# Kernel tuning notes

Measured on AMD Instinct MI355X. Metric: run time of the kernel, lower is better.

Reference implementation:

```python
import jax, jax.numpy as jnp
import numpy as np

NUM_USERS = 100000
NUM_ITEMS = 100000
EMB_DIM = 64
NUM_NODES = NUM_USERS + NUM_ITEMS
NUM_EDGES = 4000000
BATCH = 4096
NUM_LAYERS = 2


def setup_inputs() -> dict:
    key = jax.random.key(0)
    ks = jax.random.split(key, 8)
    user = jax.random.randint(ks[0], (BATCH,), 0, NUM_USERS, dtype=jnp.int64) if jax.config.jax_enable_x64 else jax.random.randint(ks[0], (BATCH,), 0, NUM_USERS, dtype=jnp.int32)
    pos = jax.random.randint(ks[1], (BATCH,), 0, NUM_ITEMS, dtype=jnp.int32)
    neg = jax.random.randint(ks[2], (BATCH,), 0, NUM_ITEMS, dtype=jnp.int32)
    edge_row = jax.random.randint(ks[3], (NUM_EDGES,), 0, NUM_NODES, dtype=jnp.int32)
    edge_col = jax.random.randint(ks[4], (NUM_EDGES,), 0, NUM_NODES, dtype=jnp.int32)
    # normalized adjacency values (degree-normalized in real LightGCN)
    edge_val = jax.random.uniform(ks[5], (NUM_EDGES,), dtype=jnp.float32) * 0.01
    user_emb = jax.random.normal(ks[6], (NUM_USERS, EMB_DIM), dtype=jnp.float32) * 0.01
    item_emb = jax.random.normal(ks[7], (NUM_ITEMS, EMB_DIM), dtype=jnp.float32) * 0.01
    return {"user": user, "pos": pos, "neg": neg,
            "edge_row": edge_row, "edge_col": edge_col, "edge_val": edge_val,
            "user_emb": user_emb, "item_emb": item_emb}


def _spmm(edge_row, edge_col, edge_val, x):
    # out[r] = sum_e val[e] * x[col[e]]  -- sparse adjacency times dense emb
    msgs = edge_val[:, None] * x[edge_col]  # [E, D]
    return jax.ops.segment_sum(msgs, edge_row, num_segments=NUM_NODES)


def reference(user, pos, neg, edge_row, edge_col, edge_val, user_emb, item_emb):
    all_emb = jnp.concatenate([user_emb, item_emb], axis=0)  # [N, D]
    acc = all_emb
    h = all_emb
    for _ in range(NUM_LAYERS):
        h = _spmm(edge_row, edge_col, edge_val, h)
        acc = acc + h
    lightgcn_out = acc / (NUM_LAYERS + 1)  # mean over stacked layer embeddings
    u = lightgcn_out[:NUM_USERS]
    i = lightgcn_out[NUM_USERS:]
    user_latent = u[user]          # [B, D]
    positive_latent = i[pos]       # [B, D]
    negative_latent = i[neg]       # [B, D]
    positive_score = jnp.sum(user_latent * positive_latent, axis=1)
    negative_score = jnp.sum(user_latent * negative_latent, axis=1)
    return positive_score, negative_score
```

## Files before the change

### kernel.cpp

```cpp
#include <hip/hip_runtime.h>
#include <cstdint>
#include <cstddef>

#define NUM_USERS 100000
#define NUM_ITEMS 100000
#define NUM_NODES 200000
#define NUM_EDGES 4000000
#define BATCH     4096
#define EMB       64

#define NB    782
#define CAP   5632
#define CHUNK 16384
#define PTHREADS 1024
#define EPB   16


__device__ __forceinline__ unsigned short f2bf(float f) {
    unsigned u = __float_as_uint(f);
    u = (u + 0x7FFFu + ((u >> 16) & 1u)) >> 16;
    return (unsigned short)u;
}
__device__ __forceinline__ float bf2f(unsigned short b) {
    return __uint_as_float(((unsigned)b) << 16);
}


__global__ void k_cvt(const float* __restrict__ uemb, const float* __restrict__ iemb,
                      unsigned short* __restrict__ xb, int* __restrict__ bcur) {
    int i = blockIdx.x * blockDim.x + threadIdx.x;
    if (i < NB) bcur[i] = i * CAP;
    const int TOT8 = (NUM_NODES * EMB) / 8;
    if (i >= TOT8) return;
    size_t off = (size_t)i * 8;
    const size_t UELEMS = (size_t)NUM_USERS * EMB;
    const float* src = (off < UELEMS) ? (uemb + off) : (iemb + (off - UELEMS));
    float4 f0 = ((const float4*)src)[0];
    float4 f1 = ((const float4*)src)[1];
    ushort4 o0 = make_ushort4(f2bf(f0.x), f2bf(f0.y), f2bf(f0.z), f2bf(f0.w));
    ushort4 o1 = make_ushort4(f2bf(f1.x), f2bf(f1.y), f2bf(f1.z), f2bf(f1.w));
    ((ushort4*)(xb + off))[0] = o0;
    ((ushort4*)(xb + off))[1] = o1;
}


__global__ void k_part1(const int* __restrict__ erow, const int* __restrict__ ecol,
                        const float* __restrict__ eval_, int* __restrict__ bcur,
                        int2* __restrict__ tmp) {
    __shared__ int hist[NB];
    __shared__ int base[NB];
    int t = threadIdx.x;
    int start = blockIdx.x * CHUNK;
    for (int i = t; i < NB; i += PTHREADS) hist[i] = 0;
    __syncthreads();
    int rows[EPB], ranks[EPB];
#pragma unroll
    for (int k = 0; k < EPB; ++k) {
        int e = start + t + k * PTHREADS;
        if (e < NUM_EDGES) {
            int r = erow[e];
            rows[k]  = r;
            ranks[k] = atomicAdd(&hist[r >> 8], 1);
        } else {
            rows[k] = -1;
        }
    }
    __syncthreads();
    for (int i = t; i < NB; i += PTHREADS) {
        int c = hist[i];
        base[i] = c ? atomicAdd(&bcur[i], c) : 0;
    }
    __syncthreads();
#pragma unroll
    for (int k = 0; k < EPB; ++k) {
        int e = start + t + k * PTHREADS;
        if (rows[k] >= 0) {
            int r   = rows[k];
            int bkt = r >> 8;
            int pos = base[bkt] + ranks[k];
            if (pos < (bkt + 1) * CAP)
                tmp[pos] = make_int2(((r & 255) << 24) | ecol[e], __float_as_int(eval_[e]));
        }
    }
}


__global__ void k_part2(const int* __restrict__ bcur, const int2* __restrict__ tmp,
                        int2* __restrict__ epack, int2* __restrict__ rowext) {
    __shared__ int cnt[256];
    __shared__ int sc[256];
    __shared__ int loc[256];
    int b = blockIdx.x, t = threadIdx.x;
    int base_row = b << 8;
    int nrows = min(256, NUM_NODES - base_row);
    int s0 = b * CAP;
    int n = min(bcur[b] - s0, CAP);
    if (t < 256) cnt[t] = 0;
    __syncthreads();
    for (int i = t; i < n; i += 512)
        atomicAdd(&cnt[((unsigned)tmp[s0 + i].x) >> 24], 1);
    __syncthreads();
    int v = 0;
    if (t < 256) { v = cnt[t]; sc[t] = v; }
    __syncthreads();
    for (int off = 1; off < 256; off <<= 1) {
        int add = 0;
        if (t < 256 && t >= off) add = sc[t - off];
        __syncthreads();
        if (t < 256 && t >= off) sc[t] += add;
        __syncthreads();
    }
    if (t < 256) {
        int cur = s0 + sc[t] - v;
        if (t < nrows) rowext[base_row + t] = make_int2(cur, v);
        loc[t] = cur;
    }
    __syncthreads();
    for (int i = t; i < n; i += 512) {
        int2 rec = tmp[s0 + i];
        int pos = atomicAdd(&loc[((unsigned)rec.x) >> 24], 1);
        epack[pos] = make_int2(rec.x & 0xFFFFFF, rec.y);
    }
}


__global__ void k_spmm1(const int2* __restrict__ rowext, const int2* __restrict__ epack,
                        const unsigned short* __restrict__ xb,
                        unsigned short* __restrict__ h1) {
    int wid  = (blockIdx.x * blockDim.x + threadIdx.x) >> 6;
    int lane = threadIdx.x & 63;
    if (wid >= NUM_NODES) return;
    int g = lane >> 4;
    int q = (lane & 15) * 4;
    int2 se = rowext[wid];
    int s = se.x, t = se.x + se.y;
    float a0 = 0.f, a1 = 0.f, a2 = 0.f, a3 = 0.f;
    for (int e = s; e < t; e += 8) {
        int eA = e + g, eB = e + 4 + g;
        int2 pA = epack[eA < t ? eA : s];
        int2 pB = epack[eB < t ? eB : s];
        float vA = (eA < t) ? __int_as_float(pA.y) : 0.f;
        float vB = (eB < t) ? __int_as_float(pB.y) : 0.f;
        ushort4 xA = *(const ushort4*)(xb + (size_t)pA.x * EMB + q);
        ushort4 xB = *(const ushort4*)(xb + (size_t)pB.x * EMB + q);
        a0 = fmaf(vA, bf2f(xA.x), a0); a1 = fmaf(vA, bf2f(xA.y), a1);
        a2 = fmaf(vA, bf2f(xA.z), a2); a3 = fmaf(vA, bf2f(xA.w), a3);
        a0 = fmaf(vB, bf2f(xB.x), a0); a1 = fmaf(vB, bf2f(xB.y), a1);
        a2 = fmaf(vB, bf2f(xB.z), a2); a3 = fmaf(vB, bf2f(xB.w), a3);
    }
    a0 += __shfl_xor(a0, 16, 64); a1 += __shfl_xor(a1, 16, 64);
    a2 += __shfl_xor(a2, 16, 64); a3 += __shfl_xor(a3, 16, 64);
    a0 += __shfl_xor(a0, 32, 64); a1 += __shfl_xor(a1, 32, 64);
    a2 += __shfl_xor(a2, 32, 64); a3 += __shfl_xor(a3, 32, 64);
    if (lane < 16) {
        ushort4 o = make_ushort4(f2bf(a0), f2bf(a1), f2bf(a2), f2bf(a3));
        *(ushort4*)(h1 + (size_t)wid * EMB + q) = o;
    }
}


__device__ __forceinline__ const float* node_ptr(int c, const float* __restrict__ uemb,
                                                 const float* __restrict__ iemb) {
    return (c < NUM_USERS) ? (uemb + (size_t)c * EMB)
                           : (iemb + (size_t)(c - NUM_USERS) * EMB);
}

__global__ void k_final(const int* __restrict__ user, const int* __restrict__ pos,
                        const int* __restrict__ neg,
                        const int2* __restrict__ rowext, const int2* __restrict__ epack,
                        const float* __restrict__ uemb, const float* __restrict__ iemb,
                        const unsigned short* __restrict__ h1, float* __restrict__ out) {
    __shared__ float lds[3 * EMB];
    int b    = blockIdx.x;
    int w    = threadIdx.x >> 6;
    int lane = threadIdx.x & 63;
    int g = lane >> 4;
    int q = (lane & 15) * 4;

    int node;
    if (w == 0)      node = user[b];
    else if (w == 1) node = NUM_USERS + pos[b];
    else             node = NUM_USERS + neg[b];

    int2 se = rowext[node];
    int s = se.x, t = se.x + se.y;
    float a0 = 0.f, a1 = 0.f, a2 = 0.f, a3 = 0.f;
    for (int e = s; e < t; e += 8) {
        int eA = e + g, eB = e + 4 + g;
        int2 pA = epack[eA < t ? eA : s];
        int2 pB = epack[eB < t ? eB : s];
        float vA = (eA < t) ? __int_as_float(pA.y) : 0.f;
        float vB = (eB < t) ? __int_as_float(pB.y) : 0.f;
        ushort4 yA = *(const ushort4*)(h1 + (size_t)pA.x * EMB + q);
        ushort4 yB = *(const ushort4*)(h1 + (size_t)pB.x * EMB + q);
        a0 = fmaf(vA, bf2f(yA.x), a0); a1 = fmaf(vA, bf2f(yA.y), a1);
        a2 = fmaf(vA, bf2f(yA.z), a2); a3 = fmaf(vA, bf2f(yA.w), a3);
        a0 = fmaf(vB, bf2f(yB.x), a0); a1 = fmaf(vB, bf2f(yB.y), a1);
        a2 = fmaf(vB, bf2f(yB.z), a2); a3 = fmaf(vB, bf2f(yB.w), a3);
    }
    a0 += __shfl_xor(a0, 16, 64); a1 += __shfl_xor(a1, 16, 64);
    a2 += __shfl_xor(a2, 16, 64); a3 += __shfl_xor(a3, 16, 64);
    a0 += __shfl_xor(a0, 32, 64); a1 += __shfl_xor(a1, 32, 64);
    a2 += __shfl_xor(a2, 32, 64); a3 += __shfl_xor(a3, 32, 64);

    if (lane < 16) {
        const float* xbp = node_ptr(node, uemb, iemb) + q;
        float4  xd = *(const float4*)xbp;
        ushort4 hn = *(const ushort4*)(h1 + (size_t)node * EMB + q);
        a0 = (a0 + xd.x + bf2f(hn.x)) / 3.0f;
        a1 = (a1 + xd.y + bf2f(hn.y)) / 3.0f;
        a2 = (a2 + xd.z + bf2f(hn.z)) / 3.0f;
        a3 = (a3 + xd.w + bf2f(hn.w)) / 3.0f;
        *(float4*)(lds + w * EMB + q) = make_float4(a0, a1, a2, a3);
    }
    __syncthreads();

    if (w < 2) {
        float prod = lds[lane] * lds[(w + 1) * EMB + lane];
        for (int off = 32; off; off >>= 1) prod += __shfl_xor(prod, off, 64);
        if (lane == 0) out[w * BATCH + b] = prod;
    }
}


extern "C" void kernel_launch(void* const* d_in, const int* in_sizes, int n_in,
                              void* d_out, int out_size, void* d_ws, size_t ws_size,
                              hipStream_t stream) {
    const int*   user  = (const int*)d_in[0];
    const int*   pos   = (const int*)d_in[1];
    const int*   neg   = (const int*)d_in[2];
    const int*   erow  = (const int*)d_in[3];
    const int*   ecol  = (const int*)d_in[4];
    const float* eval_ = (const float*)d_in[5];
    const float* uemb  = (const float*)d_in[6];
    const float* iemb  = (const float*)d_in[7];
    float* out = (float*)d_out;

    char* ws = (char*)d_ws;
    unsigned short* xb = (unsigned short*)(ws);
    unsigned short* h1 = (unsigned short*)(ws + 25600000);
    int2* tmp     = (int2*)(ws + 25600000);
    int2* rowext  = (int2*)(ws + 60833792);
    int*  bcur    = (int*)(ws + 62433792);
    int2* epack   = (int2*)(ws + 62437888);

    k_cvt<<<((NUM_NODES * EMB) / 8 + 255) / 256, 256, 0, stream>>>(uemb, iemb, xb, bcur);

    k_part1<<<(NUM_EDGES + CHUNK - 1) / CHUNK, PTHREADS, 0, stream>>>(erow, ecol, eval_,
                                                                      bcur, tmp);

    k_part2<<<NB, 512, 0, stream>>>(bcur, tmp, epack, rowext);

    k_spmm1<<<(NUM_NODES * 64 + 255) / 256, 256, 0, stream>>>(rowext, epack, xb, h1);

    k_final<<<BATCH, 192, 0, stream>>>(user, pos, neg, rowext, epack,
                                       uemb, iemb, h1, out);
}
```

Before: 352.0 us.

## Compute first-layer SpMM only for rows needed by batch neighbourhoods

The change builds bitmaps marking the batch nodes and then, during the partition pass, the neighbours of those batch nodes. The first-layer SpMM then skips every row that the final gather never reads. It also folds the bf16 conversion kernel into the partition kernel, replaces the bucket-cursor init with a memset, caches records in registers in part2, and splits off the unmasked full-8 edge loop in spmm1. The aim is to cut launches and avoid computing h1 for most of the graph. In exchange it adds a global atomicOr per edge of a marked row and extra bitmap traffic.

Result: no change. 345.2 us (-2.0%).

```diff
diff --git a/kernel.cpp b/kernel.cpp
--- a/kernel.cpp
+++ b/kernel.cpp
@@ -14,6 +14,8 @@
 #define CHUNK 16384
 #define PTHREADS 1024
 #define EPB   16
+#define RPT   11
+#define NWORDS 6250
 
 
 __device__ __forceinline__ unsigned short f2bf(float f) {
@@ -26,33 +28,42 @@
 }
 
 
-__global__ void k_cvt(const float* __restrict__ uemb, const float* __restrict__ iemb,
-                      unsigned short* __restrict__ xb, int* __restrict__ bcur) {
-    int i = blockIdx.x * blockDim.x + threadIdx.x;
-    if (i < NB) bcur[i] = i * CAP;
-    const int TOT8 = (NUM_NODES * EMB) / 8;
-    if (i >= TOT8) return;
-    size_t off = (size_t)i * 8;
-    const size_t UELEMS = (size_t)NUM_USERS * EMB;
-    const float* src = (off < UELEMS) ? (uemb + off) : (iemb + (off - UELEMS));
-    float4 f0 = ((const float4*)src)[0];
-    float4 f1 = ((const float4*)src)[1];
-    ushort4 o0 = make_ushort4(f2bf(f0.x), f2bf(f0.y), f2bf(f0.z), f2bf(f0.w));
-    ushort4 o1 = make_ushort4(f2bf(f1.x), f2bf(f1.y), f2bf(f1.z), f2bf(f1.w));
-    ((ushort4*)(xb + off))[0] = o0;
-    ((ushort4*)(xb + off))[1] = o1;
-}
-
-
-__global__ void k_part1(const int* __restrict__ erow, const int* __restrict__ ecol,
-                        const float* __restrict__ eval_, int* __restrict__ bcur,
+__global__ void k_part1(const int* __restrict__ user, const int* __restrict__ pos,
+                        const int* __restrict__ neg,
+                        const int* __restrict__ erow, const int* __restrict__ ecol,
+                        const float* __restrict__ eval_,
+                        const float* __restrict__ uemb, const float* __restrict__ iemb,
+                        unsigned short* __restrict__ xb,
+                        int* __restrict__ bcur,
+                        unsigned* __restrict__ memb, unsigned* __restrict__ need,
                         int2* __restrict__ tmp) {
     __shared__ int hist[NB];
     __shared__ int base[NB];
     int t = threadIdx.x;
+    int gid = blockIdx.x * PTHREADS + t;
+    for (int i = t; i < NB; i += PTHREADS) hist[i] = 0;
+
+    const int TOT8 = (NUM_NODES * EMB) / 8;
+    const size_t UELEMS = (size_t)NUM_USERS * EMB;
+    for (int i = gid; i < TOT8; i += gridDim.x * PTHREADS) {
+        size_t off = (size_t)i * 8;
+        const float* src = (off < UELEMS) ? (uemb + off) : (iemb + (off - UELEMS));
+        float4 f0 = ((const float4*)src)[0];
+        float4 f1 = ((const float4*)src)[1];
+        ((ushort4*)(xb + off))[0] = make_ushort4(f2bf(f0.x), f2bf(f0.y), f2bf(f0.z), f2bf(f0.w));
+        ((ushort4*)(xb + off))[1] = make_ushort4(f2bf(f1.x), f2bf(f1.y), f2bf(f1.z), f2bf(f1.w));
+    }
+    if (gid < 3 * BATCH) {
+        int b = gid & (BATCH - 1);
+        int w = gid >> 12;
+        int node = (w == 0) ? user[b] : (w == 1) ? (NUM_USERS + pos[b]) : (NUM_USERS + neg[b]);
+        unsigned bit = 1u << (node & 31);
+        atomicOr(&memb[node >> 5], bit);
+        atomicOr(&need[node >> 5], bit);
+    }
+    __syncthreads();
+
     int start = blockIdx.x * CHUNK;
-    for (int i = t; i < NB; i += PTHREADS) hist[i] = 0;
-    __syncthreads();
     int rows[EPB], ranks[EPB];
 #pragma unroll
     for (int k = 0; k < EPB; ++k) {
@@ -77,28 +88,42 @@
         if (rows[k] >= 0) {
             int r   = rows[k];
             int bkt = r >> 8;
-            int pos = base[bkt] + ranks[k];
-            if (pos < (bkt + 1) * CAP)
-                tmp[pos] = make_int2(((r & 255) << 24) | ecol[e], __float_as_int(eval_[e]));
+            int rel = base[bkt] + ranks[k];
+            if (rel < CAP)
+                tmp[bkt * CAP + rel] = make_int2(((r & 255) << 24) | ecol[e], __float_as_int(eval_[e]));
         }
     }
 }
 
 
 __global__ void k_part2(const int* __restrict__ bcur, const int2* __restrict__ tmp,
-                        int2* __restrict__ epack, int2* __restrict__ rowext) {
+                        const unsigned* __restrict__ memb,
+                        int2* __restrict__ epack, int2* __restrict__ rowext,
+                        unsigned* __restrict__ need) {
     __shared__ int cnt[256];
     __shared__ int sc[256];
     __shared__ int loc[256];
+    __shared__ unsigned mw[8];
     int b = blockIdx.x, t = threadIdx.x;
     int base_row = b << 8;
     int nrows = min(256, NUM_NODES - base_row);
     int s0 = b * CAP;
-    int n = min(bcur[b] - s0, CAP);
+    int n = min(bcur[b], CAP);
     if (t < 256) cnt[t] = 0;
-    __syncthreads();
-    for (int i = t; i < n; i += 512)
-        atomicAdd(&cnt[((unsigned)tmp[s0 + i].x) >> 24], 1);
+    if (t < 8) {
+        int wi = (base_row >> 5) + t;
+        mw[t] = (wi < NWORDS) ? memb[wi] : 0u;
+    }
+    __syncthreads();
+    int2 r[RPT];
+#pragma unroll
+    for (int i = 0; i < RPT; ++i) {
+        int idx = t + i * 512;
+        if (idx < n) {
+            r[i] = tmp[s0 + idx];
+            atomicAdd(&cnt[((unsigned)r[i].x) >> 24], 1);
+        }
+    }
     __syncthreads();
     int v = 0;
     if (t < 256) { v = cnt[t]; sc[t] = v; }
@@ -116,26 +141,50 @@
         loc[t] = cur;
     }
     __syncthreads();
-    for (int i = t; i < n; i += 512) {
-        int2 rec = tmp[s0 + i];
-        int pos = atomicAdd(&loc[((unsigned)rec.x) >> 24], 1);
-        epack[pos] = make_int2(rec.x & 0xFFFFFF, rec.y);
+#pragma unroll
+    for (int i = 0; i < RPT; ++i) {
+        int idx = t + i * 512;
+        if (idx < n) {
+            int2 rec = r[i];
+            unsigned rl = ((unsigned)rec.x) >> 24;
+            int p = atomicAdd(&loc[rl], 1);
+            int col = rec.x & 0xFFFFFF;
+            epack[p] = make_int2(col, rec.y);
+            if ((mw[rl >> 5] >> (rl & 31)) & 1u)
+                atomicOr(&need[col >> 5], 1u << (col & 31));
+        }
     }
 }
 
 
 __global__ void k_spmm1(const int2* __restrict__ rowext, const int2* __restrict__ epack,
                         const unsigned short* __restrict__ xb,
+                        const unsigned* __restrict__ need,
                         unsigned short* __restrict__ h1) {
     int wid  = (blockIdx.x * blockDim.x + threadIdx.x) >> 6;
     int lane = threadIdx.x & 63;
     if (wid >= NUM_NODES) return;
+    if (!((need[wid >> 5] >> (wid & 31)) & 1u)) return;
     int g = lane >> 4;
     int q = (lane & 15) * 4;
     int2 se = rowext[wid];
     int s = se.x, t = se.x + se.y;
     float a0 = 0.f, a1 = 0.f, a2 = 0.f, a3 = 0.f;
-    for (int e = s; e < t; e += 8) {
+    int e = s;
+    int tfull = s + ((t - s) & ~7);
+    for (; e < tfull; e += 8) {
+        int2 pA = epack[e + g];
+        int2 pB = epack[e + 4 + g];
+        float vA = __int_as_float(pA.y);
+        float vB = __int_as_float(pB.y);
+        ushort4 xA = *(const ushort4*)(xb + (size_t)pA.x * EMB + q);
+        ushort4 xB = *(const ushort4*)(xb + (size_t)pB.x * EMB + q);
+        a0 = fmaf(vA, bf2f(xA.x), a0); a1 = fmaf(vA, bf2f(xA.y), a1);
+        a2 = fmaf(vA, bf2f(xA.z), a2); a3 = fmaf(vA, bf2f(xA.w), a3);
+        a0 = fmaf(vB, bf2f(xB.x), a0); a1 = fmaf(vB, bf2f(xB.y), a1);
+        a2 = fmaf(vB, bf2f(xB.z), a2); a3 = fmaf(vB, bf2f(xB.w), a3);
+    }
+    if (e < t) {
         int eA = e + g, eB = e + 4 + g;
         int2 pA = epack[eA < t ? eA : s];
         int2 pB = epack[eB < t ? eB : s];
@@ -239,19 +288,21 @@
     char* ws = (char*)d_ws;
     unsigned short* xb = (unsigned short*)(ws);
     unsigned short* h1 = (unsigned short*)(ws + 25600000);
-    int2* tmp     = (int2*)(ws + 25600000);
-    int2* rowext  = (int2*)(ws + 60833792);
-    int*  bcur    = (int*)(ws + 62433792);
-    int2* epack   = (int2*)(ws + 62437888);
-
-    k_cvt<<<((NUM_NODES * EMB) / 8 + 255) / 256, 256, 0, stream>>>(uemb, iemb, xb, bcur);
-
-    k_part1<<<(NUM_EDGES + CHUNK - 1) / CHUNK, PTHREADS, 0, stream>>>(erow, ecol, eval_,
-                                                                      bcur, tmp);
-
-    k_part2<<<NB, 512, 0, stream>>>(bcur, tmp, epack, rowext);
-
-    k_spmm1<<<(NUM_NODES * 64 + 255) / 256, 256, 0, stream>>>(rowext, epack, xb, h1);
+    int2* tmp      = (int2*)(ws + 25600000);
+    int2* rowext   = (int2*)(ws + 60833792);
+    int*  bcur     = (int*)(ws + 62433792);
+    unsigned* memb = (unsigned*)(ws + 62436920);
+    unsigned* need = (unsigned*)(ws + 62461920);
+    int2* epack    = (int2*)(ws + 62486920);
+
+    hipMemsetAsync(ws + 62433792, 0, 53128, stream);
+
+    k_part1<<<(NUM_EDGES + CHUNK - 1) / CHUNK, PTHREADS, 0, stream>>>(
+        user, pos, neg, erow, ecol, eval_, uemb, iemb, xb, bcur, memb, need, tmp);
+
+    k_part2<<<NB, 512, 0, stream>>>(bcur, tmp, memb, epack, rowext, need);
+
+    k_spmm1<<<(NUM_NODES * 64 + 255) / 256, 256, 0, stream>>>(rowext, epack, xb, need, h1);
 
     k_final<<<BATCH, 192, 0, stream>>>(user, pos, neg, rowext, epack,
                                        uemb, iemb, h1, out);
```
